# Performance work log

Hardware: AMD Instinct MI355X
Metric: run time of the kernel (lower is better)

The kernel has to match this reference:

```python
import jax, jax.numpy as jnp
import numpy as np

H = 16          # heads_num
D = 1024        # model_dim
HD = D // H     # per-head dim
NEG = -1e9


def setup_inputs() -> dict:
    key = jax.random.key(0)
    ks = jax.random.split(key, 12)
    B, S = 4, 1024
    inp = {
        "q": jax.random.normal(ks[0], (B, S, D), jnp.float32),
        "k": jax.random.normal(ks[1], (B, S, D), jnp.float32),
        "v": jax.random.normal(ks[2], (B, S, D), jnp.float32),
        "mask": jnp.ones((B, 1, S), jnp.int32),
    }
    s = 1.0 / np.sqrt(D)
    inp["Wq"] = jax.random.normal(ks[3], (D, D), jnp.float32) * s
    inp["bq"] = jnp.zeros((D,), jnp.float32)
    inp["Wk"] = jax.random.normal(ks[4], (D, D), jnp.float32) * s
    inp["bk"] = jnp.zeros((D,), jnp.float32)
    inp["Wv"] = jax.random.normal(ks[5], (D, D), jnp.float32) * s
    inp["bv"] = jnp.zeros((D,), jnp.float32)
    inp["Wo"] = jax.random.normal(ks[6], (D, D), jnp.float32) * s
    inp["bo"] = jnp.zeros((D,), jnp.float32)
    return inp


def _split_heads(x, B):
    # [B, S, D] -> [B, H, S, HD]
    return x.reshape(B, -1, H, HD).transpose(0, 2, 1, 3)


def reference(q, k, v, mask, Wq, bq, Wk, bk, Wv, bv, Wo, bo):
    B = q.shape[0]
    qh = _split_heads(q @ Wq.T + bq, B)  # [B,H,Sq,HD]
    kh = _split_heads(k @ Wk.T + bk, B)  # [B,H,Sk,HD]
    vh = _split_heads(v @ Wv.T + bv, B)  # [B,H,Sk,HD]
    scores = jnp.einsum("bhqd,bhkd->bhqk", qh, kh) / np.sqrt(HD)
    # mask [B,1,Sk] -> unsqueeze head dim -> [B,1,1,Sk], broadcast over q and heads
    scores = jnp.where(mask[:, None] == 0, NEG, scores)
    attn = jax.nn.softmax(scores, axis=-1)  # dropout in eval mode = identity
    ctx = jnp.einsum("bhqk,bhkd->bhqd", attn, vh)
    out = ctx.transpose(0, 2, 1, 3).reshape(B, -1, D)
    return out @ Wo.T + bo
```

## Files before the change

kernel.cpp:

```cpp
#include <hip/hip_runtime.h>
#include <hip/hip_bf16.h>
#include <math.h>

typedef __bf16 bf16;
typedef __bf16 bf16x8 __attribute__((ext_vector_type(8)));
typedef __bf16 bf16x2 __attribute__((ext_vector_type(2)));
typedef float f32x4 __attribute__((ext_vector_type(4)));
typedef float f32x16 __attribute__((ext_vector_type(16)));

#define D_MODEL 1024
#define SEQ 1024
#define BATCH 4
#define NHEAD 16
#define MTOT (BATCH*SEQ)

#define QSCALE 0.18033688011112042f
#define MASKNEG -1e9f

__global__ void cast_all(const float* __restrict__ s0, const float* __restrict__ s1,
                         const float* __restrict__ s2, const float* __restrict__ s3,
                         const float* __restrict__ s4, const float* __restrict__ s5,
                         const float* __restrict__ s6,
                         bf16* d0, bf16* d1, bf16* d2, bf16* d3, bf16* d4, bf16* d5, bf16* d6) {
    int z = blockIdx.y;
    const float* s; bf16* d; int n;
    switch (z) {
        case 0: s = s0; d = d0; n = MTOT * D_MODEL; break;
        case 1: s = s1; d = d1; n = MTOT * D_MODEL; break;
        case 2: s = s2; d = d2; n = MTOT * D_MODEL; break;
        case 3: s = s3; d = d3; n = D_MODEL * D_MODEL; break;
        case 4: s = s4; d = d4; n = D_MODEL * D_MODEL; break;
        case 5: s = s5; d = d5; n = D_MODEL * D_MODEL; break;
        default: s = s6; d = d6; n = D_MODEL * D_MODEL; break;
    }
    int idx = (blockIdx.x * blockDim.x + threadIdx.x) * 8;
    int stride = gridDim.x * blockDim.x * 8;
    for (int i = idx; i < n; i += stride) {
        const float4* p = (const float4*)(s + i);
        float4 a = p[0], b = p[1];
        bf16x8 o;
        o[0] = (bf16)a.x; o[1] = (bf16)a.y; o[2] = (bf16)a.z; o[3] = (bf16)a.w;
        o[4] = (bf16)b.x; o[5] = (bf16)b.y; o[6] = (bf16)b.z; o[7] = (bf16)b.w;
        *(bf16x8*)(d + i) = o;
    }
}

template<typename OT, int MODE>
__global__ __launch_bounds__(256, 3)
void gemm_bt(const bf16* __restrict__ A0, const bf16* __restrict__ A1, const bf16* __restrict__ A2,
             const bf16* __restrict__ W0, const bf16* __restrict__ W1, const bf16* __restrict__ W2,
             const float* __restrict__ bias0, const float* __restrict__ bias1, const float* __restrict__ bias2,
             OT* __restrict__ O0, OT* __restrict__ O1, OT* __restrict__ O2) {
    constexpr int BK = 32;
    constexpr int K = D_MODEL;
    constexpr int NT = K / BK;
    __shared__ alignas(16) bf16 As[2][128 * BK];
    __shared__ alignas(16) bf16 Bs[2][128 * BK];

    int z = (MODE == 0) ? blockIdx.z : 0;
    const bf16* A = (z == 0) ? A0 : (z == 1) ? A1 : A2;
    const bf16* W = (z == 0) ? W0 : (z == 1) ? W1 : W2;
    const float* bias = (z == 0) ? bias0 : (z == 1) ? bias1 : bias2;
    OT* Out = (z == 0) ? O0 : (z == 1) ? O1 : O2;

    int tid = threadIdx.x;
    int lane = tid & 63, w = tid >> 6;
    int l15 = lane & 15, l4 = lane >> 4;
    int m0 = blockIdx.x * 128;
    int n0 = blockIdx.y * 128;
    int wm = w >> 1, wn = w & 1;

    f32x4 acc[4][4] = {};

    int srow = lane >> 2;
    int scol = (lane & 3) * 8;

    auto stage = [&](int buf, int kt) {
#pragma unroll
        for (int i = 0; i < 2; ++i) {
            int seg = w * 2 + i;
            int row = seg * 16 + srow;
            const bf16* srcA = A + (size_t)(m0 + row) * K + kt * BK + scol;
            const bf16* srcB = W + (size_t)(n0 + row) * K + kt * BK + scol;
            __builtin_amdgcn_global_load_lds(
                (const __attribute__((address_space(1))) void*)srcA,
                (__attribute__((address_space(3))) void*)(&As[buf][seg * 512]), 16, 0, 0);
            __builtin_amdgcn_global_load_lds(
                (const __attribute__((address_space(1))) void*)srcB,
                (__attribute__((address_space(3))) void*)(&Bs[buf][seg * 512]), 16, 0, 0);
        }
    };

    stage(0, 0);
    __syncthreads();

    for (int kt = 0; kt < NT; ++kt) {
        int cur = kt & 1;
        if (kt + 1 < NT) stage(cur ^ 1, kt + 1);

        const bf16* pa = &As[cur][(wm * 64 + l15) * BK + l4 * 8];
        const bf16* pb = &Bs[cur][(wn * 64 + l15) * BK + l4 * 8];
        bf16x8 af[4], bv[4];
#pragma unroll
        for (int m = 0; m < 4; ++m) af[m] = *(const bf16x8*)(pa + m * 16 * BK);
#pragma unroll
        for (int n = 0; n < 4; ++n) bv[n] = *(const bf16x8*)(pb + n * 16 * BK);
#pragma unroll
        for (int m = 0; m < 4; ++m)
#pragma unroll
            for (int n = 0; n < 4; ++n)
                acc[m][n] = __builtin_amdgcn_mfma_f32_16x16x32_bf16(af[m], bv[n], acc[m][n], 0, 0, 0);

        __syncthreads();
    }

    float bload[4];
#pragma unroll
    for (int n = 0; n < 4; ++n) bload[n] = bias[n0 + wn * 64 + n * 16 + l15];

    if (MODE == 0 && z == 2) {
#pragma unroll
        for (int m = 0; m < 4; ++m) {
            int row = m0 + wm * 64 + m * 16 + l4 * 4;
#pragma unroll
            for (int n = 0; n < 4; ++n) {
                int col = n0 + wn * 64 + n * 16 + l15;
                float bl = bload[n];
#pragma unroll
                for (int r = 0; r < 4; ++r) {
                    float vv = acc[m][n][r] + bl;
                    int rr = row + r;
                    int bb = rr >> 10, s = rr & 1023;
                    Out[((size_t)(bb * 1024 + col)) * 1024 + s] = (OT)vv;
                }
            }
        }
    } else {
        const float sc = (MODE == 0 && z == 0) ? QSCALE : 1.0f;
#pragma unroll
        for (int m = 0; m < 4; ++m) {
            int row = m0 + wm * 64 + m * 16 + l4 * 4;
#pragma unroll
            for (int n = 0; n < 4; ++n) {
                int col = n0 + wn * 64 + n * 16 + l15;
                float bl = bload[n];
#pragma unroll
                for (int r = 0; r < 4; ++r) {
                    float vv = (acc[m][n][r] + bl) * sc;
                    Out[(size_t)(row + r) * D_MODEL + col] = (OT)vv;
                }
            }
        }
    }
}

__device__ __forceinline__ unsigned pkbf(float lo, float hi2) {
    bf16x2 t; t[0] = (bf16)lo; t[1] = (bf16)hi2;
    return __builtin_bit_cast(unsigned, t);
}

__global__ __launch_bounds__(512, 2)
void attn_fwd(const bf16* __restrict__ Qp, const bf16* __restrict__ Kp,
              const bf16* __restrict__ VT, const int* __restrict__ maskp,
              bf16* __restrict__ ctx) {
    __shared__ alignas(16) bf16 Kls[2][64 * 64];
    __shared__ alignas(16) bf16 Vls[2][64 * 64];
    __shared__ alignas(16) float madd2[SEQ];
    __shared__ int tflag[16];

    int tid = threadIdx.x;
    int lane = tid & 63, w = tid >> 6;
    int l31 = lane & 31, hi = lane >> 5;

    int fid = blockIdx.x;
    int xcd = fid & 7, idx = fid >> 3;
    int by = xcd * 8 + (idx >> 2);
    int bx = idx & 3;
    int b = by >> 4, h = by & 15;
    int q0 = bx * 256;

    {
        int m0v = maskp[b * SEQ + tid];
        int m1v = maskp[b * SEQ + 512 + tid];
        madd2[tid] = m0v ? 0.f : MASKNEG;
        madd2[512 + tid] = m1v ? 0.f : MASKNEG;
        unsigned long long b0 = __ballot(m0v != 0);
        unsigned long long b1 = __ballot(m1v != 0);
        if (lane == 0) {
            tflag[w] = (b0 == ~0ull);
            tflag[8 + w] = (b1 == ~0ull);
        }
    }

    bf16x8 qf[4];
    {
        const bf16* qb = Qp + ((size_t)(b * SEQ + q0 + w * 32 + l31)) * D_MODEL + h * 64 + hi * 8;
#pragma unroll
        for (int ks = 0; ks < 4; ++ks) qf[ks] = *(const bf16x8*)(qb + ks * 16);
    }

    f32x16 oacc0 = {}, oacc1 = {};
    float lsum = 0.f;

    auto stage = [&](int buf, int kt) {
        int kv0 = kt * 64;
        int row = w * 8 + (lane >> 3);
        int cs = ((lane & 7) ^ (row & 7)) * 8;
        const bf16* srcK = Kp + ((size_t)(b * SEQ + kv0 + row)) * D_MODEL + h * 64 + cs;
        __builtin_amdgcn_global_load_lds(
            (const __attribute__((address_space(1))) void*)srcK,
            (__attribute__((address_space(3))) void*)(&Kls[buf][w * 512]), 16, 0, 0);
        const bf16* srcV = VT + ((size_t)(b * 1024 + h * 64 + row)) * SEQ + kv0 + cs;
        __builtin_amdgcn_global_load_lds(
            (const __attribute__((address_space(1))) void*)srcV,
            (__attribute__((address_space(3))) void*)(&Vls[buf][w * 512]), 16, 0, 0);
    };

    stage(0, 0);
    __syncthreads();

    for (int kt = 0; kt < SEQ / 64; ++kt) {
        int cur = kt & 1;
        if (kt + 1 < SEQ / 64) stage(cur ^ 1, kt + 1);

        f32x16 p0 = {}, p1 = {};
        __builtin_amdgcn_s_setprio(1);
#pragma unroll
        for (int ks = 0; ks < 4; ++ks) {
            int slot = ((2 * ks + hi) ^ (l31 & 7)) * 8;
            bf16x8 k0 = *(const bf16x8*)(&Kls[cur][l31 * 64 + slot]);
            bf16x8 k1 = *(const bf16x8*)(&Kls[cur][(32 + l31) * 64 + slot]);
            p0 = __builtin_amdgcn_mfma_f32_32x32x16_bf16(k0, qf[ks], p0, 0, 0, 0);
            p1 = __builtin_amdgcn_mfma_f32_32x32x16_bf16(k1, qf[ks], p1, 0, 0, 0);
        }
        __builtin_amdgcn_s_setprio(0);

        float a0 = 0.f, a1 = 0.f, a2 = 0.f, a3 = 0.f;
        if (tflag[kt]) {
#pragma unroll
            for (int g = 0; g < 4; ++g) {
                float s0 = 0.f, s1 = 0.f;
#pragma unroll
                for (int c = 0; c < 4; ++c) {
                    int r = g * 4 + c;
                    float e0 = exp2f(p0[r]);
                    float e1 = exp2f(p1[r]);
                    p0[r] = e0; p1[r] = e1;
                    s0 += e0; s1 += e1;
                }
                if (g == 0) a0 = s0 + s1;
                else if (g == 1) a1 = s0 + s1;
                else if (g == 2) a2 = s0 + s1;
                else a3 = s0 + s1;
            }
        } else {
            const float* mb = &madd2[kt * 64];
#pragma unroll
            for (int g = 0; g < 4; ++g) {
                f32x4 mk0 = *(const f32x4*)(mb + g * 8 + hi * 4);
                f32x4 mk1 = *(const f32x4*)(mb + 32 + g * 8 + hi * 4);
                float s0 = 0.f, s1 = 0.f;
#pragma unroll
                for (int c = 0; c < 4; ++c) {
                    int r = g * 4 + c;
                    float e0 = exp2f(p0[r] + mk0[c]);
                    float e1 = exp2f(p1[r] + mk1[c]);
                    p0[r] = e0; p1[r] = e1;
                    s0 += e0; s1 += e1;
                }
                if (g == 0) a0 = s0 + s1;
                else if (g == 1) a1 = s0 + s1;
                else if (g == 2) a2 = s0 + s1;
                else a3 = s0 + s1;
            }
        }
        float acc_s = (a0 + a1) + (a2 + a3);
        acc_s += __shfl_xor(acc_s, 32);
        lsum += acc_s;

        union FragU { bf16x8 v; unsigned u[4]; };
        FragU pa0, pa1, pa2, pa3;
#define PKSW(PV, RA, RB, DST)  { \
            unsigned a_ = pkbf(PV[RA], PV[(RA) + 1]); \
            unsigned b_ = pkbf(PV[RB], PV[(RB) + 1]); \
            auto rr_ = __builtin_amdgcn_permlane32_swap(a_, b_, false, false); \
            DST.u[((RA) & 3) >> 1] = rr_[0]; DST.u[(((RA) & 3) >> 1) + 2] = rr_[1]; }
        PKSW(p0, 0, 4,  pa0);
        PKSW(p0, 2, 6,  pa0);
        PKSW(p0, 8, 12, pa1);
        PKSW(p0, 10, 14, pa1);
        PKSW(p1, 0, 4,  pa2);
        PKSW(p1, 2, 6,  pa2);
        PKSW(p1, 8, 12, pa3);
        PKSW(p1, 10, 14, pa3);
#undef PKSW

        __builtin_amdgcn_s_setprio(1);
#pragma unroll
        for (int ks = 0; ks < 4; ++ks) {
            bf16x8 pav = (ks == 0) ? pa0.v : (ks == 1) ? pa1.v : (ks == 2) ? pa2.v : pa3.v;
            int slot = ((2 * ks + hi) ^ (l31 & 7)) * 8;
            bf16x8 v0 = *(const bf16x8*)(&Vls[cur][l31 * 64 + slot]);
            bf16x8 v1 = *(const bf16x8*)(&Vls[cur][(32 + l31) * 64 + slot]);
            oacc0 = __builtin_amdgcn_mfma_f32_32x32x16_bf16(pav, v0, oacc0, 0, 0, 0);
            oacc1 = __builtin_amdgcn_mfma_f32_32x32x16_bf16(pav, v1, oacc1, 0, 0, 0);
        }
        __builtin_amdgcn_s_setprio(0);

        __syncthreads();
    }

#pragma unroll
    for (int g = 0; g < 4; ++g) {
#pragma unroll
        for (int c = 0; c < 4; ++c) {
            int r = g * 4 + c;
            int qloc = c + g * 8 + hi * 4;
            float sden = __shfl(lsum, qloc);
            float inv = 1.0f / sden;
            int qg = q0 + w * 32 + qloc;
            size_t base = ((size_t)(b * SEQ + qg)) * D_MODEL + h * 64;
            ctx[base + l31]      = (bf16)(oacc0[r] * inv);
            ctx[base + 32 + l31] = (bf16)(oacc1[r] * inv);
        }
    }
}

extern "C" void kernel_launch(void* const* d_in, const int* in_sizes, int n_in,
                              void* d_out, int out_size, void* d_ws, size_t ws_size,
                              hipStream_t stream) {
    const float* q  = (const float*)d_in[0];
    const float* k  = (const float*)d_in[1];
    const float* v  = (const float*)d_in[2];
    const int* mask = (const int*)d_in[3];
    const float* Wq = (const float*)d_in[4];
    const float* bq = (const float*)d_in[5];
    const float* Wk = (const float*)d_in[6];
    const float* bk = (const float*)d_in[7];
    const float* Wv = (const float*)d_in[8];
    const float* bv = (const float*)d_in[9];
    const float* Wo = (const float*)d_in[10];
    const float* bo = (const float*)d_in[11];
    float* out = (float*)d_out;

    char* ws = (char*)d_ws;
    size_t szQKV = (size_t)MTOT * D_MODEL * sizeof(bf16);
    size_t szW = (size_t)D_MODEL * D_MODEL * sizeof(bf16);
    bf16* qb  = (bf16*)ws; ws += szQKV;
    bf16* kb  = (bf16*)ws; ws += szQKV;
    bf16* vb  = (bf16*)ws; ws += szQKV;
    bf16* Wqb = (bf16*)ws; ws += szW;
    bf16* Wkb = (bf16*)ws; ws += szW;
    bf16* Wvb = (bf16*)ws; ws += szW;
    bf16* Wob = (bf16*)ws; ws += szW;
    bf16* Qp  = (bf16*)ws; ws += szQKV;
    bf16* Kp  = (bf16*)ws; ws += szQKV;
    bf16* VT  = (bf16*)ws; ws += szQKV;
    bf16* ctx = (bf16*)ws; ws += szQKV;

    dim3 gc(512, 7, 1);
    cast_all<<<gc, 256, 0, stream>>>(q, k, v, Wq, Wk, Wv, Wo,
                                     qb, kb, vb, Wqb, Wkb, Wvb, Wob);

    dim3 g1(MTOT / 128, D_MODEL / 128, 3);
    gemm_bt<bf16, 0><<<g1, 256, 0, stream>>>(qb, kb, vb, Wqb, Wkb, Wvb,
                                             bq, bk, bv, Qp, Kp, VT);

    attn_fwd<<<dim3(256), 512, 0, stream>>>(Qp, Kp, VT, mask, ctx);

    dim3 g3(MTOT / 128, D_MODEL / 128, 1);
    gemm_bt<float, 1><<<g3, 256, 0, stream>>>(ctx, ctx, ctx, Wob, Wob, Wob,
                                              bo, bo, bo, out, out, out);
}
```

Before: 114.2 us.

## Use 128-query blocks with 4 waves and 128-key tiles in attention

The attention kernel now launches 512 blocks of 256 threads (4 waves, 128 queries each) instead of 256 blocks of 512 threads. Each pipeline step stages a 128-key tile of K and V with a 16-slot XOR swizzle for V, and processes it as two 64-key halves. This halves the number of barriers per block and doubles the number of blocks to improve load balance across CUs. In exchange, LDS per block roughly doubles, which may limit how many blocks fit on a CU, and K/V are re-read by twice as many blocks.

New measurement: 111.8 us. 2.1% less time.

```diff
diff --git a/kernel.cpp b/kernel.cpp
--- a/kernel.cpp
+++ b/kernel.cpp
@@ -159,12 +159,12 @@
     return __builtin_bit_cast(unsigned, t);
 }
 
-__global__ __launch_bounds__(512, 2)
+__global__ __launch_bounds__(256, 2)
 void attn_fwd(const bf16* __restrict__ Qp, const bf16* __restrict__ Kp,
               const bf16* __restrict__ VT, const int* __restrict__ maskp,
               bf16* __restrict__ ctx) {
-    __shared__ alignas(16) bf16 Kls[2][64 * 64];
-    __shared__ alignas(16) bf16 Vls[2][64 * 64];
+    __shared__ alignas(16) bf16 Kls[2][128 * 64];
+    __shared__ alignas(16) bf16 Vls[2][64 * 128];
     __shared__ alignas(16) float madd2[SEQ];
     __shared__ int tflag[16];
 
@@ -174,21 +174,22 @@
 
     int fid = blockIdx.x;
     int xcd = fid & 7, idx = fid >> 3;
-    int by = xcd * 8 + (idx >> 2);
-    int bx = idx & 3;
+    int by = xcd * 8 + (idx >> 3);
+    int bx = idx & 7;
     int b = by >> 4, h = by & 15;
-    int q0 = bx * 256;
+    int q0 = bx * 128;
 
     {
-        int m0v = maskp[b * SEQ + tid];
-        int m1v = maskp[b * SEQ + 512 + tid];
-        madd2[tid] = m0v ? 0.f : MASKNEG;
-        madd2[512 + tid] = m1v ? 0.f : MASKNEG;
-        unsigned long long b0 = __ballot(m0v != 0);
-        unsigned long long b1 = __ballot(m1v != 0);
-        if (lane == 0) {
-            tflag[w] = (b0 == ~0ull);
-            tflag[8 + w] = (b1 == ~0ull);
+#pragma unroll
+        for (int i = 0; i < 4; ++i) {
+            int pos = tid + i * 256;
+            madd2[pos] = maskp[b * SEQ + pos] ? 0.f : MASKNEG;
+        }
+#pragma unroll
+        for (int i = 0; i < 4; ++i) {
+            int t = w * 4 + i;
+            unsigned long long bl = __ballot(maskp[b * SEQ + t * 64 + lane] != 0);
+            if (lane == 0) tflag[t] = (bl == ~0ull);
         }
     }
 
@@ -203,40 +204,42 @@
     float lsum = 0.f;
 
     auto stage = [&](int buf, int kt) {
-        int kv0 = kt * 64;
-        int row = w * 8 + (lane >> 3);
-        int cs = ((lane & 7) ^ (row & 7)) * 8;
-        const bf16* srcK = Kp + ((size_t)(b * SEQ + kv0 + row)) * D_MODEL + h * 64 + cs;
-        __builtin_amdgcn_global_load_lds(
-            (const __attribute__((address_space(1))) void*)srcK,
-            (__attribute__((address_space(3))) void*)(&Kls[buf][w * 512]), 16, 0, 0);
-        const bf16* srcV = VT + ((size_t)(b * 1024 + h * 64 + row)) * SEQ + kv0 + cs;
-        __builtin_amdgcn_global_load_lds(
-            (const __attribute__((address_space(1))) void*)srcV,
-            (__attribute__((address_space(3))) void*)(&Vls[buf][w * 512]), 16, 0, 0);
+        int kv0 = kt * 128;
+#pragma unroll
+        for (int i = 0; i < 4; ++i) {
+            int row = w * 32 + i * 8 + (lane >> 3);
+            int cs = ((lane & 7) ^ (row & 7)) * 8;
+            const bf16* srcK = Kp + ((size_t)(b * SEQ + kv0 + row)) * D_MODEL + h * 64 + cs;
+            __builtin_amdgcn_global_load_lds(
+                (const __attribute__((address_space(1))) void*)srcK,
+                (__attribute__((address_space(3))) void*)(&Kls[buf][(w * 32 + i * 8) * 64]), 16, 0, 0);
+        }
+#pragma unroll
+        for (int j = 0; j < 4; ++j) {
+            int row = w * 16 + j * 4 + (lane >> 4);
+            int cs = ((lane & 15) ^ (row & 15)) * 8;
+            const bf16* srcV = VT + ((size_t)(b * 1024 + h * 64 + row)) * SEQ + kv0 + cs;
+            __builtin_amdgcn_global_load_lds(
+                (const __attribute__((address_space(1))) void*)srcV,
+                (__attribute__((address_space(3))) void*)(&Vls[buf][(w * 16 + j * 4) * 128]), 16, 0, 0);
+        }
     };
 
-    stage(0, 0);
-    __syncthreads();
-
-    for (int kt = 0; kt < SEQ / 64; ++kt) {
-        int cur = kt & 1;
-        if (kt + 1 < SEQ / 64) stage(cur ^ 1, kt + 1);
-
+    auto half = [&](int cur, int krb, int ksb, int flag, const float* mb) {
         f32x16 p0 = {}, p1 = {};
         __builtin_amdgcn_s_setprio(1);
 #pragma unroll
         for (int ks = 0; ks < 4; ++ks) {
-            int slot = ((2 * ks + hi) ^ (l31 & 7)) * 8;
-            bf16x8 k0 = *(const bf16x8*)(&Kls[cur][l31 * 64 + slot]);
-            bf16x8 k1 = *(const bf16x8*)(&Kls[cur][(32 + l31) * 64 + slot]);
+            int sl = ((2 * ks + hi) ^ (l31 & 7)) * 8;
+            bf16x8 k0 = *(const bf16x8*)(&Kls[cur][(krb + l31) * 64 + sl]);
+            bf16x8 k1 = *(const bf16x8*)(&Kls[cur][(krb + 32 + l31) * 64 + sl]);
             p0 = __builtin_amdgcn_mfma_f32_32x32x16_bf16(k0, qf[ks], p0, 0, 0, 0);
             p1 = __builtin_amdgcn_mfma_f32_32x32x16_bf16(k1, qf[ks], p1, 0, 0, 0);
         }
         __builtin_amdgcn_s_setprio(0);
 
         float a0 = 0.f, a1 = 0.f, a2 = 0.f, a3 = 0.f;
-        if (tflag[kt]) {
+        if (flag) {
 #pragma unroll
             for (int g = 0; g < 4; ++g) {
                 float s0 = 0.f, s1 = 0.f;
@@ -254,7 +257,6 @@
                 else a3 = s0 + s1;
             }
         } else {
-            const float* mb = &madd2[kt * 64];
 #pragma unroll
             for (int g = 0; g < 4; ++g) {
                 f32x4 mk0 = *(const f32x4*)(mb + g * 8 + hi * 4);
@@ -297,15 +299,28 @@
 
         __builtin_amdgcn_s_setprio(1);
 #pragma unroll
-        for (int ks = 0; ks < 4; ++ks) {
-            bf16x8 pav = (ks == 0) ? pa0.v : (ks == 1) ? pa1.v : (ks == 2) ? pa2.v : pa3.v;
-            int slot = ((2 * ks + hi) ^ (l31 & 7)) * 8;
-            bf16x8 v0 = *(const bf16x8*)(&Vls[cur][l31 * 64 + slot]);
-            bf16x8 v1 = *(const bf16x8*)(&Vls[cur][(32 + l31) * 64 + slot]);
+        for (int i = 0; i < 4; ++i) {
+            int ks = ksb + i;
+            bf16x8 pav = (i == 0) ? pa0.v : (i == 1) ? pa1.v : (i == 2) ? pa2.v : pa3.v;
+            int sl = ((2 * ks + hi) ^ (l31 & 15)) * 8;
+            bf16x8 v0 = *(const bf16x8*)(&Vls[cur][l31 * 128 + sl]);
+            bf16x8 v1 = *(const bf16x8*)(&Vls[cur][(32 + l31) * 128 + sl]);
             oacc0 = __builtin_amdgcn_mfma_f32_32x32x16_bf16(pav, v0, oacc0, 0, 0, 0);
             oacc1 = __builtin_amdgcn_mfma_f32_32x32x16_bf16(pav, v1, oacc1, 0, 0, 0);
         }
         __builtin_amdgcn_s_setprio(0);
+    };
+
+    stage(0, 0);
+    __syncthreads();
+
+    for (int kt = 0; kt < SEQ / 128; ++kt) {
+        int cur = kt & 1;
+        if (kt + 1 < SEQ / 128) stage(cur ^ 1, kt + 1);
+
+        const float* mb = &madd2[kt * 128];
+        half(cur, 0,  0, tflag[2 * kt],     mb);
+        half(cur, 64, 4, tflag[2 * kt + 1], mb + 64);
 
         __syncthreads();
     }
@@ -366,7 +381,7 @@
     gemm_bt<bf16, 0><<<g1, 256, 0, stream>>>(qb, kb, vb, Wqb, Wkb, Wvb,
                                              bq, bk, bv, Qp, Kp, VT);
 
-    attn_fwd<<<dim3(256), 512, 0, stream>>>(Qp, Kp, VT, mask, ctx);
+    attn_fwd<<<dim3(512), 256, 0, stream>>>(Qp, Kp, VT, mask, ctx);
 
     dim3 g3(MTOT / 128, D_MODEL / 128, 1);
     gemm_bt<float, 1><<<g3, 256, 0, stream>>>(ctx, ctx, ctx, Wob, Wob, Wob,
```
